# Kernel tuning notes

Measured on AMD Instinct MI355X. Metric: run time of the kernel, lower is better.

## Reference

```python
import jax, jax.numpy as jnp
import numpy as np

B, T, N, C, H = 32, 50, 1024, 128, 64


def setup_inputs() -> dict:
    key = jax.random.key(0)
    ks = jax.random.split(key, 5)
    s_ih = 1.0 / np.sqrt(H)
    return {
        "chars": jax.random.normal(ks[0], (B, T, N, C), dtype=jnp.float32),
        "W_ih": jax.random.uniform(ks[1], (3 * H, C), minval=-s_ih, maxval=s_ih, dtype=jnp.float32),
        "W_hh": jax.random.uniform(ks[2], (3 * H, H), minval=-s_ih, maxval=s_ih, dtype=jnp.float32),
        "b_ih": jax.random.uniform(ks[3], (3 * H,), minval=-s_ih, maxval=s_ih, dtype=jnp.float32),
        "b_hh": jax.random.uniform(ks[4], (3 * H,), minval=-s_ih, maxval=s_ih, dtype=jnp.float32),
    }


def _gru_scan(chars, W_ih, W_hh, b_ih, b_hh):
    b, t, n, c = chars.shape
    h_dim = W_hh.shape[1]
    # (B,T,N,C) -> (T, B*N, C): every (batch, stock) pair is an independent sequence
    x = jnp.transpose(chars, (1, 0, 2, 3)).reshape(t, b * n, c)
    # precompute input projections for all steps: (T, B*N, 3H)
    gi = jnp.einsum("tbc,gc->tbg", x, W_ih) + b_ih

    def step(h, gi_t):
        gh = h @ W_hh.T + b_hh                      # (B*N, 3H)
        i_r, i_z, i_n = jnp.split(gi_t, 3, axis=-1)
        h_r, h_z, h_n = jnp.split(gh, 3, axis=-1)
        r = jax.nn.sigmoid(i_r + h_r)
        z = jax.nn.sigmoid(i_z + h_z)
        nn_ = jnp.tanh(i_n + r * h_n)
        h_new = (1.0 - z) * nn_ + z * h
        return h_new, None

    h0 = jnp.zeros((b * n, h_dim), dtype=chars.dtype)
    h_final, _ = jax.lax.scan(step, h0, gi)
    return h_final.reshape(b, n, h_dim)


def reference(chars, W_ih, W_hh, b_ih, b_hh):
    return _gru_scan(chars, W_ih, W_hh, b_ih, b_hh)
```

## Files before the change

### kernel.cpp

```cpp
#include <hip/hip_runtime.h>


typedef _Float16 half8 __attribute__((ext_vector_type(8)));
typedef float f32x4 __attribute__((ext_vector_type(4)));

constexpr int T_ = 50, N_ = 1024, C_ = 128, H_ = 64;
constexpr int WIH_OFF = 0;
constexpr int WHH_OFF = 49152;
constexpr int H_OFF   = 73728;
constexpr int LDS_BYTES = 90112;

__global__ void prep_weights(const float* __restrict__ Wih, const float* __restrict__ Whh,
                             _Float16* __restrict__ w16) {
  int i = blockIdx.x * 256 + threadIdx.x;
  if (i < 192 * 128) w16[i] = (_Float16)Wih[i];
  if (i < 192 * 64)  w16[24576 + i] = (_Float16)Whh[i];
}

__global__ __launch_bounds__(512, 2) void gru_mfma(
    const float* __restrict__ x, const _Float16* __restrict__ w16,
    const float* __restrict__ bih, const float* __restrict__ bhh,
    float* __restrict__ out)
{
  __shared__ __align__(16) char lds[LDS_BYTES];
  const int tid = threadIdx.x;

  {
    const _Float16* wih = w16;
    const _Float16* whh = w16 + 24576;
#pragma unroll
    for (int rep = 0; rep < 6; ++rep) {
      int i = tid + rep * 512;
      int row = i >> 4;
      uint32_t byte = ((uint32_t)i << 4) ^ ((row & 7) << 4);
      *(half8*)(lds + WIH_OFF + byte) = *(const half8*)(wih + i * 8);
    }
#pragma unroll
    for (int rep = 0; rep < 3; ++rep) {
      int i = tid + rep * 512;
      int row = i >> 3;
      uint32_t byte = ((uint32_t)i << 4) ^ ((row & 7) << 4);
      *(half8*)(lds + WHH_OFF + byte) = *(const half8*)(whh + i * 8);
    }
    half8 zz = {};
#pragma unroll
    for (int rep = 0; rep < 2; ++rep)
      *(half8*)(lds + H_OFF + (tid + rep * 512) * 16) = zz;
  }
  __syncthreads();

  const int wv = tid >> 6, lane = tid & 63;
  const int c = lane & 15, g = lane >> 4;
  const uint32_t hbase = H_OFF + wv * 2048;
  const int gseq0 = blockIdx.x * 128 + wv * 16;
  const int b = gseq0 >> 10, n0 = gseq0 & (N_ - 1);
  const float* xrow = x + ((size_t)b * T_ * N_ + n0 + c) * C_;
  const size_t stepstride = (size_t)N_ * C_;

  float br[4], bz[4], bin[4], bhn[4];
#pragma unroll
  for (int j4 = 0; j4 < 4; ++j4) {
    int j = j4 * 16 + c;
    br[j4]  = bih[j] + bhh[j];
    bz[j4]  = bih[64 + j] + bhh[64 + j];
    bin[j4] = bih[128 + j];
    bhn[j4] = bhh[128 + j];
  }

  float hreg[16];
#pragma unroll
  for (int i = 0; i < 16; ++i) hreg[i] = 0.f;

  float4 raw[8];
#pragma unroll
  for (int ks = 0; ks < 4; ++ks)
#pragma unroll
    for (int hf = 0; hf < 2; ++hf)
      raw[ks * 2 + hf] = *(const float4*)(xrow + ks * 32 + g * 8 + hf * 4);

  for (int t = 0; t < T_; ++t) {
    half8 xf[4];
#pragma unroll
    for (int ks = 0; ks < 4; ++ks) {
      const float4 lo = raw[ks * 2], hi = raw[ks * 2 + 1];
      xf[ks][0] = (_Float16)lo.x; xf[ks][1] = (_Float16)lo.y;
      xf[ks][2] = (_Float16)lo.z; xf[ks][3] = (_Float16)lo.w;
      xf[ks][4] = (_Float16)hi.x; xf[ks][5] = (_Float16)hi.y;
      xf[ks][6] = (_Float16)hi.z; xf[ks][7] = (_Float16)hi.w;
    }
    {
      const int tn = (t + 1 < T_) ? t + 1 : T_ - 1;
      const float* xp = xrow + (size_t)tn * stepstride;
#pragma unroll
      for (int ks = 0; ks < 4; ++ks)
#pragma unroll
        for (int hf = 0; hf < 2; ++hf)
          raw[ks * 2 + hf] = *(const float4*)(xp + ks * 32 + g * 8 + hf * 4);
    }

    f32x4 Orz[8], Oin[4], Ohn[4];
#pragma unroll
    for (int i = 0; i < 8; ++i) Orz[i] = (f32x4){0.f, 0.f, 0.f, 0.f};
#pragma unroll
    for (int i = 0; i < 4; ++i) { Oin[i] = (f32x4){0.f, 0.f, 0.f, 0.f};
                                  Ohn[i] = (f32x4){0.f, 0.f, 0.f, 0.f}; }

#pragma unroll
    for (int ks = 0; ks < 4; ++ks) {
      const half8 a = xf[ks];
#pragma unroll
      for (int ct = 0; ct < 8; ++ct) {
        const int row = ct * 16 + c;
        const uint32_t byte = (uint32_t)(WIH_OFF + row * 256 + ks * 64 + g * 16) ^ ((row & 7) << 4);
        Orz[ct] = __builtin_amdgcn_mfma_f32_16x16x32_f16(a, *(const half8*)(lds + byte), Orz[ct], 0, 0, 0);
      }
#pragma unroll
      for (int ct = 0; ct < 4; ++ct) {
        const int row = 128 + ct * 16 + c;
        const uint32_t byte = (uint32_t)(WIH_OFF + row * 256 + ks * 64 + g * 16) ^ ((row & 7) << 4);
        Oin[ct] = __builtin_amdgcn_mfma_f32_16x16x32_f16(a, *(const half8*)(lds + byte), Oin[ct], 0, 0, 0);
      }
    }
#pragma unroll
    for (int ks2 = 0; ks2 < 2; ++ks2) {
      const uint32_t abyte = (hbase + c * 128 + ks2 * 64 + g * 16) ^ ((c & 7) << 4);
      const half8 a = *(const half8*)(lds + abyte);
#pragma unroll
      for (int ct = 0; ct < 8; ++ct) {
        const int row = ct * 16 + c;
        const uint32_t byte = (uint32_t)(WHH_OFF + row * 128 + ks2 * 64 + g * 16) ^ ((row & 7) << 4);
        Orz[ct] = __builtin_amdgcn_mfma_f32_16x16x32_f16(a, *(const half8*)(lds + byte), Orz[ct], 0, 0, 0);
      }
#pragma unroll
      for (int ct = 0; ct < 4; ++ct) {
        const int row = 128 + ct * 16 + c;
        const uint32_t byte = (uint32_t)(WHH_OFF + row * 128 + ks2 * 64 + g * 16) ^ ((row & 7) << 4);
        Ohn[ct] = __builtin_amdgcn_mfma_f32_16x16x32_f16(a, *(const half8*)(lds + byte), Ohn[ct], 0, 0, 0);
      }
    }

#pragma unroll
    for (int v = 0; v < 4; ++v) {
#pragma unroll
      for (int j4 = 0; j4 < 4; ++j4) {
        const float rp = Orz[j4][v] + br[j4];
        const float zp = Orz[4 + j4][v] + bz[j4];
        const float r = __builtin_amdgcn_rcpf(1.f + __expf(-rp));
        const float z = __builtin_amdgcn_rcpf(1.f + __expf(-zp));
        const float np = Oin[j4][v] + bin[j4] + r * (Ohn[j4][v] + bhn[j4]);
        const float nn = 1.f - 2.f * __builtin_amdgcn_rcpf(__expf(2.f * np) + 1.f);
        const float hn = (1.f - z) * nn + z * hreg[v * 4 + j4];
        hreg[v * 4 + j4] = hn;
        const int s = g * 4 + v;
        const uint32_t byte = (hbase + s * 128 + (j4 * 16 + c) * 2) ^ ((s & 7) << 4);
        *(_Float16*)(lds + byte) = (_Float16)hn;
      }
    }
  }

#pragma unroll
  for (int v = 0; v < 4; ++v) {
    const int s = g * 4 + v;
#pragma unroll
    for (int j4 = 0; j4 < 4; ++j4)
      out[(size_t)(gseq0 + s) * H_ + j4 * 16 + c] = hreg[v * 4 + j4];
  }
}

extern "C" void kernel_launch(void* const* d_in, const int* in_sizes, int n_in,
                              void* d_out, int out_size, void* d_ws, size_t ws_size,
                              hipStream_t stream) {
  const float* chars = (const float*)d_in[0];
  const float* Wih   = (const float*)d_in[1];
  const float* Whh   = (const float*)d_in[2];
  const float* bih   = (const float*)d_in[3];
  const float* bhh   = (const float*)d_in[4];

  _Float16* w16 = (_Float16*)d_ws;

  prep_weights<<<144, 256, 0, stream>>>(Wih, Whh, w16);
  gru_mfma<<<256, 512, 0, stream>>>(chars, w16, bih, bhh, (float*)d_out);
}
```

Before: 252.6 us.

## Switch GRU kernel to 32x32x16 MFMA tiles with W_hh held in registers

Replaces the 16x16x32 MFMA tiling with 32x32x16 MFMAs, so each wave handles 32 sequences. The recurrent weight W_hh moves from LDS into per-lane registers, and the LDS swizzle changes to a 16-way XOR. Blocks shrink to 256 threads with launch bounds of one block per CU, and the next-step input prefetch is placed between MFMA groups. The aim is fewer LDS reads per FLOP and more reuse per instruction, at the cost of higher register pressure and fewer resident waves to hide latency.

```diff
diff --git a/kernel.cpp b/kernel.cpp
--- a/kernel.cpp
+++ b/kernel.cpp
@@ -2,13 +2,12 @@
 
 
 typedef _Float16 half8 __attribute__((ext_vector_type(8)));
-typedef float f32x4 __attribute__((ext_vector_type(4)));
+typedef float f32x16 __attribute__((ext_vector_type(16)));
 
 constexpr int T_ = 50, N_ = 1024, C_ = 128, H_ = 64;
 constexpr int WIH_OFF = 0;
-constexpr int WHH_OFF = 49152;
-constexpr int H_OFF   = 73728;
-constexpr int LDS_BYTES = 90112;
+constexpr int H_OFF   = 49152;
+constexpr int LDS_BYTES = 81920;
 
 __global__ void prep_weights(const float* __restrict__ Wih, const float* __restrict__ Whh,
                              _Float16* __restrict__ w16) {
@@ -17,7 +16,11 @@
   if (i < 192 * 64)  w16[24576 + i] = (_Float16)Whh[i];
 }
 
-__global__ __launch_bounds__(512, 2) void gru_mfma(
+__device__ __forceinline__ float sigm(float x) {
+  return __builtin_amdgcn_rcpf(1.f + __expf(-x));
+}
+
+__global__ __launch_bounds__(256, 1) void gru_mfma32(
     const float* __restrict__ x, const _Float16* __restrict__ w16,
     const float* __restrict__ bih, const float* __restrict__ bhh,
     float* __restrict__ out)
@@ -27,144 +30,161 @@
 
   {
     const _Float16* wih = w16;
-    const _Float16* whh = w16 + 24576;
-#pragma unroll
-    for (int rep = 0; rep < 6; ++rep) {
-      int i = tid + rep * 512;
-      int row = i >> 4;
-      uint32_t byte = ((uint32_t)i << 4) ^ ((row & 7) << 4);
+#pragma unroll
+    for (int rep = 0; rep < 12; ++rep) {
+      int i = tid + rep * 256;
+      int row = i >> 4, gr = i & 15;
+      uint32_t byte = (uint32_t)row * 256 + (uint32_t)((gr ^ (row & 15)) << 4);
       *(half8*)(lds + WIH_OFF + byte) = *(const half8*)(wih + i * 8);
     }
-#pragma unroll
-    for (int rep = 0; rep < 3; ++rep) {
-      int i = tid + rep * 512;
-      int row = i >> 3;
-      uint32_t byte = ((uint32_t)i << 4) ^ ((row & 7) << 4);
-      *(half8*)(lds + WHH_OFF + byte) = *(const half8*)(whh + i * 8);
-    }
     half8 zz = {};
 #pragma unroll
-    for (int rep = 0; rep < 2; ++rep)
-      *(half8*)(lds + H_OFF + (tid + rep * 512) * 16) = zz;
+    for (int rep = 0; rep < 8; ++rep)
+      *(half8*)(lds + H_OFF + tid * 128 + rep * 16) = zz;
   }
   __syncthreads();
 
   const int wv = tid >> 6, lane = tid & 63;
-  const int c = lane & 15, g = lane >> 4;
-  const uint32_t hbase = H_OFF + wv * 2048;
-  const int gseq0 = blockIdx.x * 128 + wv * 16;
+  const int c32 = lane & 31, hf = lane >> 5;
+  const int sw15 = c32 & 15;
+  const uint32_t hbase = H_OFF + wv * 8192;
+  const int gseq0 = blockIdx.x * 128 + wv * 32;
   const int b = gseq0 >> 10, n0 = gseq0 & (N_ - 1);
-  const float* xrow = x + ((size_t)b * T_ * N_ + n0 + c) * C_;
+
+  const _Float16* whh = w16 + 24576;
+  half8 wf[6][4];
+#pragma unroll
+  for (int ct = 0; ct < 6; ++ct)
+#pragma unroll
+    for (int ks = 0; ks < 4; ++ks)
+      wf[ct][ks] = *(const half8*)(whh + (ct * 32 + c32) * 64 + ks * 16 + hf * 8);
+
+  float br[2], bz[2], bin_[2], bhn_[2];
+#pragma unroll
+  for (int jj = 0; jj < 2; ++jj) {
+    int j = jj * 32 + c32;
+    br[jj]   = bih[j] + bhh[j];
+    bz[jj]   = bih[64 + j] + bhh[64 + j];
+    bin_[jj] = bih[128 + j];
+    bhn_[jj] = bhh[128 + j];
+  }
+
+  float hr[32];
+#pragma unroll
+  for (int i = 0; i < 32; ++i) hr[i] = 0.f;
+
+  const float* xlane = x + ((size_t)b * T_ * N_ + n0 + c32) * C_ + hf * 8;
   const size_t stepstride = (size_t)N_ * C_;
 
-  float br[4], bz[4], bin[4], bhn[4];
-#pragma unroll
-  for (int j4 = 0; j4 < 4; ++j4) {
-    int j = j4 * 16 + c;
-    br[j4]  = bih[j] + bhh[j];
-    bz[j4]  = bih[64 + j] + bhh[64 + j];
-    bin[j4] = bih[128 + j];
-    bhn[j4] = bhh[128 + j];
-  }
-
-  float hreg[16];
-#pragma unroll
-  for (int i = 0; i < 16; ++i) hreg[i] = 0.f;
-
-  float4 raw[8];
-#pragma unroll
-  for (int ks = 0; ks < 4; ++ks)
-#pragma unroll
-    for (int hf = 0; hf < 2; ++hf)
-      raw[ks * 2 + hf] = *(const float4*)(xrow + ks * 32 + g * 8 + hf * 4);
+#define WIHB(gt, ks) \
+  (*(const half8*)(lds + WIH_OFF + (uint32_t)(((gt) * 32 + c32) * 256) + \
+                   (uint32_t)(((((ks) * 2 + hf) ^ sw15)) << 4)))
+#define MFMA(a, bfrag, acc) __builtin_amdgcn_mfma_f32_32x32x16_f16((a), (bfrag), (acc), 0, 0, 0)
+
+  float4 raw[16];
+#pragma unroll
+  for (int ks = 0; ks < 8; ++ks) {
+    raw[ks * 2]     = *(const float4*)(xlane + ks * 16);
+    raw[ks * 2 + 1] = *(const float4*)(xlane + ks * 16 + 4);
+  }
 
   for (int t = 0; t < T_; ++t) {
-    half8 xf[4];
+    half8 xf[8];
+#pragma unroll
+    for (int ks = 0; ks < 8; ++ks) {
+      const float4 lo = raw[ks * 2], hi = raw[ks * 2 + 1];
+      half8 v;
+      v[0] = (_Float16)lo.x; v[1] = (_Float16)lo.y;
+      v[2] = (_Float16)lo.z; v[3] = (_Float16)lo.w;
+      v[4] = (_Float16)hi.x; v[5] = (_Float16)hi.y;
+      v[6] = (_Float16)hi.z; v[7] = (_Float16)hi.w;
+      xf[ks] = v;
+    }
+
+    half8 ha[4];
 #pragma unroll
     for (int ks = 0; ks < 4; ++ks) {
-      const float4 lo = raw[ks * 2], hi = raw[ks * 2 + 1];
-      xf[ks][0] = (_Float16)lo.x; xf[ks][1] = (_Float16)lo.y;
-      xf[ks][2] = (_Float16)lo.z; xf[ks][3] = (_Float16)lo.w;
-      xf[ks][4] = (_Float16)hi.x; xf[ks][5] = (_Float16)hi.y;
-      xf[ks][6] = (_Float16)hi.z; xf[ks][7] = (_Float16)hi.w;
-    }
+      uint32_t byte = hbase + (uint32_t)(c32 * 256) + (uint32_t)(((ks * 2 + hf) ^ sw15) << 4);
+      ha[ks] = *(const half8*)(lds + byte);
+    }
+
+    f32x16 aR0 = {}, aZ0 = {}, aN0 = {}, aH0 = {};
+    f32x16 aR1 = {}, aZ1 = {}, aN1 = {}, aH1 = {};
+
+#pragma unroll
+    for (int ks = 0; ks < 8; ++ks) aR0 = MFMA(xf[ks], WIHB(0, ks), aR0);
+#pragma unroll
+    for (int ks = 0; ks < 8; ++ks) aZ0 = MFMA(xf[ks], WIHB(2, ks), aZ0);
+#pragma unroll
+    for (int ks = 0; ks < 8; ++ks) aN0 = MFMA(xf[ks], WIHB(4, ks), aN0);
+#pragma unroll
+    for (int ks = 0; ks < 4; ++ks) aR0 = MFMA(ha[ks], wf[0][ks], aR0);
+#pragma unroll
+    for (int ks = 0; ks < 4; ++ks) aZ0 = MFMA(ha[ks], wf[2][ks], aZ0);
+#pragma unroll
+    for (int ks = 0; ks < 4; ++ks) aH0 = MFMA(ha[ks], wf[4][ks], aH0);
+
+#pragma unroll
+    for (int ks = 0; ks < 8; ++ks) aR1 = MFMA(xf[ks], WIHB(1, ks), aR1);
+#pragma unroll
+    for (int ks = 0; ks < 8; ++ks) aZ1 = MFMA(xf[ks], WIHB(3, ks), aZ1);
+#pragma unroll
+    for (int ks = 0; ks < 8; ++ks) aN1 = MFMA(xf[ks], WIHB(5, ks), aN1);
+
     {
       const int tn = (t + 1 < T_) ? t + 1 : T_ - 1;
-      const float* xp = xrow + (size_t)tn * stepstride;
-#pragma unroll
-      for (int ks = 0; ks < 4; ++ks)
-#pragma unroll
-        for (int hf = 0; hf < 2; ++hf)
-          raw[ks * 2 + hf] = *(const float4*)(xp + ks * 32 + g * 8 + hf * 4);
-    }
-
-    f32x4 Orz[8], Oin[4], Ohn[4];
-#pragma unroll
-    for (int i = 0; i < 8; ++i) Orz[i] = (f32x4){0.f, 0.f, 0.f, 0.f};
-#pragma unroll
-    for (int i = 0; i < 4; ++i) { Oin[i] = (f32x4){0.f, 0.f, 0.f, 0.f};
-                                  Ohn[i] = (f32x4){0.f, 0.f, 0.f, 0.f}; }
-
-#pragma unroll
-    for (int ks = 0; ks < 4; ++ks) {
-      const half8 a = xf[ks];
-#pragma unroll
-      for (int ct = 0; ct < 8; ++ct) {
-        const int row = ct * 16 + c;
-        const uint32_t byte = (uint32_t)(WIH_OFF + row * 256 + ks * 64 + g * 16) ^ ((row & 7) << 4);
-        Orz[ct] = __builtin_amdgcn_mfma_f32_16x16x32_f16(a, *(const half8*)(lds + byte), Orz[ct], 0, 0, 0);
+      const float* xp = xlane + (size_t)tn * stepstride;
+#pragma unroll
+      for (int ks = 0; ks < 8; ++ks) {
+        raw[ks * 2]     = *(const float4*)(xp + ks * 16);
+        raw[ks * 2 + 1] = *(const float4*)(xp + ks * 16 + 4);
       }
-#pragma unroll
-      for (int ct = 0; ct < 4; ++ct) {
-        const int row = 128 + ct * 16 + c;
-        const uint32_t byte = (uint32_t)(WIH_OFF + row * 256 + ks * 64 + g * 16) ^ ((row & 7) << 4);
-        Oin[ct] = __builtin_amdgcn_mfma_f32_16x16x32_f16(a, *(const half8*)(lds + byte), Oin[ct], 0, 0, 0);
-      }
-    }
-#pragma unroll
-    for (int ks2 = 0; ks2 < 2; ++ks2) {
-      const uint32_t abyte = (hbase + c * 128 + ks2 * 64 + g * 16) ^ ((c & 7) << 4);
-      const half8 a = *(const half8*)(lds + abyte);
-#pragma unroll
-      for (int ct = 0; ct < 8; ++ct) {
-        const int row = ct * 16 + c;
-        const uint32_t byte = (uint32_t)(WHH_OFF + row * 128 + ks2 * 64 + g * 16) ^ ((row & 7) << 4);
-        Orz[ct] = __builtin_amdgcn_mfma_f32_16x16x32_f16(a, *(const half8*)(lds + byte), Orz[ct], 0, 0, 0);
-      }
-#pragma unroll
-      for (int ct = 0; ct < 4; ++ct) {
-        const int row = 128 + ct * 16 + c;
-        const uint32_t byte = (uint32_t)(WHH_OFF + row * 128 + ks2 * 64 + g * 16) ^ ((row & 7) << 4);
-        Ohn[ct] = __builtin_amdgcn_mfma_f32_16x16x32_f16(a, *(const half8*)(lds + byte), Ohn[ct], 0, 0, 0);
-      }
-    }
-
-#pragma unroll
-    for (int v = 0; v < 4; ++v) {
-#pragma unroll
-      for (int j4 = 0; j4 < 4; ++j4) {
-        const float rp = Orz[j4][v] + br[j4];
-        const float zp = Orz[4 + j4][v] + bz[j4];
-        const float r = __builtin_amdgcn_rcpf(1.f + __expf(-rp));
-        const float z = __builtin_amdgcn_rcpf(1.f + __expf(-zp));
-        const float np = Oin[j4][v] + bin[j4] + r * (Ohn[j4][v] + bhn[j4]);
-        const float nn = 1.f - 2.f * __builtin_amdgcn_rcpf(__expf(2.f * np) + 1.f);
-        const float hn = (1.f - z) * nn + z * hreg[v * 4 + j4];
-        hreg[v * 4 + j4] = hn;
-        const int s = g * 4 + v;
-        const uint32_t byte = (hbase + s * 128 + (j4 * 16 + c) * 2) ^ ((s & 7) << 4);
-        *(_Float16*)(lds + byte) = (_Float16)hn;
-      }
-    }
-  }
-
-#pragma unroll
-  for (int v = 0; v < 4; ++v) {
-    const int s = g * 4 + v;
-#pragma unroll
-    for (int j4 = 0; j4 < 4; ++j4)
-      out[(size_t)(gseq0 + s) * H_ + j4 * 16 + c] = hreg[v * 4 + j4];
-  }
+    }
+
+#pragma unroll
+    for (int ks = 0; ks < 4; ++ks) aR1 = MFMA(ha[ks], wf[1][ks], aR1);
+#pragma unroll
+    for (int ks = 0; ks < 4; ++ks) aZ1 = MFMA(ha[ks], wf[3][ks], aZ1);
+#pragma unroll
+    for (int ks = 0; ks < 4; ++ks) aH1 = MFMA(ha[ks], wf[5][ks], aH1);
+
+#pragma unroll
+    for (int rg = 0; rg < 16; ++rg) {
+      const int seq = (rg & 3) + 8 * (rg >> 2) + 4 * hf;
+      const float r = sigm(aR0[rg] + br[0]);
+      const float z = sigm(aZ0[rg] + bz[0]);
+      const float np = aN0[rg] + bin_[0] + r * (aH0[rg] + bhn_[0]);
+      const float nn = 1.f - 2.f * __builtin_amdgcn_rcpf(__expf(2.f * np) + 1.f);
+      const float hn = (1.f - z) * nn + z * hr[rg];
+      hr[rg] = hn;
+      const uint32_t gr = (uint32_t)((0 * 4 + (c32 >> 3)) ^ (seq & 15));
+      const uint32_t byte = hbase + (uint32_t)(seq * 256) + (gr << 4) + (uint32_t)((c32 * 2) & 15);
+      *(_Float16*)(lds + byte) = (_Float16)hn;
+    }
+#pragma unroll
+    for (int rg = 0; rg < 16; ++rg) {
+      const int seq = (rg & 3) + 8 * (rg >> 2) + 4 * hf;
+      const float r = sigm(aR1[rg] + br[1]);
+      const float z = sigm(aZ1[rg] + bz[1]);
+      const float np = aN1[rg] + bin_[1] + r * (aH1[rg] + bhn_[1]);
+      const float nn = 1.f - 2.f * __builtin_amdgcn_rcpf(__expf(2.f * np) + 1.f);
+      const float hn = (1.f - z) * nn + z * hr[16 + rg];
+      hr[16 + rg] = hn;
+      const uint32_t gr = (uint32_t)((1 * 4 + (c32 >> 3)) ^ (seq & 15));
+      const uint32_t byte = hbase + (uint32_t)(seq * 256) + (gr << 4) + (uint32_t)((c32 * 2) & 15);
+      *(_Float16*)(lds + byte) = (_Float16)hn;
+    }
+  }
+
+#pragma unroll
+  for (int jj = 0; jj < 2; ++jj)
+#pragma unroll
+    for (int rg = 0; rg < 16; ++rg) {
+      const int seq = (rg & 3) + 8 * (rg >> 2) + 4 * hf;
+      out[(size_t)(gseq0 + seq) * H_ + jj * 32 + c32] = hr[jj * 16 + rg];
+    }
+#undef WIHB
+#undef MFMA
 }
 
 extern "C" void kernel_launch(void* const* d_in, const int* in_sizes, int n_in,
@@ -179,5 +199,5 @@
   _Float16* w16 = (_Float16*)d_ws;
 
   prep_weights<<<144, 256, 0, stream>>>(Wih, Whh, w16);
-  gru_mfma<<<256, 512, 0, stream>>>(chars, w16, bih, bhh, (float*)d_out);
-}
+  gru_mfma32<<<256, 256, 0, stream>>>(chars, w16, bih, bhh, (float*)d_out);
+}
```

Measured after the change: 231.7 us. 8.3% less time.

## Keep W_hh fragments in registers and halve block size for GRU kernel

Applied to the files above, without the earlier changes.

Loads the recurrent weight matrix W_hh once per wave into register-resident half8 fragments instead of re-reading it from LDS every timestep. This shrinks LDS per block so the kernel can run as 512 blocks of 256 threads, each covering 64 sequences. The per-step LDS traffic on the serial recurrence path should drop. The cost is much higher VGPR pressure, which could cause spills or limit occupancy.

```diff
diff --git a/kernel.cpp b/kernel.cpp
--- a/kernel.cpp
+++ b/kernel.cpp
@@ -5,10 +5,9 @@
 typedef float f32x4 __attribute__((ext_vector_type(4)));
 
 constexpr int T_ = 50, N_ = 1024, C_ = 128, H_ = 64;
-constexpr int WIH_OFF = 0;
-constexpr int WHH_OFF = 49152;
-constexpr int H_OFF   = 73728;
-constexpr int LDS_BYTES = 90112;
+constexpr uint32_t WIH_OFF = 0;
+constexpr uint32_t HT_OFF  = 49152;
+constexpr int LDS_BYTES = 57344;
 
 __global__ void prep_weights(const float* __restrict__ Wih, const float* __restrict__ Whh,
                              _Float16* __restrict__ w16) {
@@ -17,7 +16,11 @@
   if (i < 192 * 64)  w16[24576 + i] = (_Float16)Whh[i];
 }
 
-__global__ __launch_bounds__(512, 2) void gru_mfma(
+__device__ __forceinline__ float sigm(float x) {
+  return __builtin_amdgcn_rcpf(1.f + __expf(-x));
+}
+
+__global__ __launch_bounds__(256, 2) void gru_tlp(
     const float* __restrict__ x, const _Float16* __restrict__ w16,
     const float* __restrict__ bih, const float* __restrict__ bhh,
     float* __restrict__ out)
@@ -26,145 +29,144 @@
   const int tid = threadIdx.x;
 
   {
-    const _Float16* wih = w16;
-    const _Float16* whh = w16 + 24576;
 #pragma unroll
-    for (int rep = 0; rep < 6; ++rep) {
-      int i = tid + rep * 512;
+    for (int rep = 0; rep < 12; ++rep) {
+      int i = tid + rep * 256;
       int row = i >> 4;
-      uint32_t byte = ((uint32_t)i << 4) ^ ((row & 7) << 4);
-      *(half8*)(lds + WIH_OFF + byte) = *(const half8*)(wih + i * 8);
-    }
-#pragma unroll
-    for (int rep = 0; rep < 3; ++rep) {
-      int i = tid + rep * 512;
-      int row = i >> 3;
-      uint32_t byte = ((uint32_t)i << 4) ^ ((row & 7) << 4);
-      *(half8*)(lds + WHH_OFF + byte) = *(const half8*)(whh + i * 8);
+      uint32_t byte = ((uint32_t)i << 4) ^ ((uint32_t)(row & 7) << 4);
+      *(half8*)(lds + WIH_OFF + byte) = *(const half8*)(w16 + i * 8);
     }
     half8 zz = {};
-#pragma unroll
-    for (int rep = 0; rep < 2; ++rep)
-      *(half8*)(lds + H_OFF + (tid + rep * 512) * 16) = zz;
+    *(half8*)(lds + HT_OFF + tid * 32)      = zz;
+    *(half8*)(lds + HT_OFF + tid * 32 + 16) = zz;
   }
   __syncthreads();
 
   const int wv = tid >> 6, lane = tid & 63;
   const int c = lane & 15, g = lane >> 4;
-  const uint32_t hbase = H_OFF + wv * 2048;
-  const int gseq0 = blockIdx.x * 128 + wv * 16;
-  const int b = gseq0 >> 10, n0 = gseq0 & (N_ - 1);
-  const float* xrow = x + ((size_t)b * T_ * N_ + n0 + c) * C_;
-  const size_t stepstride = (size_t)N_ * C_;
+  const int sw7 = c & 7;
+  const uint32_t ht = HT_OFF + (uint32_t)wv * 2048;
+  const int seq0 = blockIdx.x * 64 + wv * 16;
+  const int b = seq0 >> 10, n0 = seq0 & (N_ - 1);
 
-  float br[4], bz[4], bin[4], bhn[4];
+  const _Float16* whh = w16 + 24576;
+  half8 wf[12][2];
+#pragma unroll
+  for (int jt = 0; jt < 12; ++jt)
+#pragma unroll
+    for (int ks2 = 0; ks2 < 2; ++ks2)
+      wf[jt][ks2] = *(const half8*)(whh + (jt * 16 + c) * 64 + ks2 * 32 + g * 8);
+
+  float br[4], bz[4], bin_[4], bhn_[4];
 #pragma unroll
   for (int j4 = 0; j4 < 4; ++j4) {
     int j = j4 * 16 + c;
-    br[j4]  = bih[j] + bhh[j];
-    bz[j4]  = bih[64 + j] + bhh[64 + j];
-    bin[j4] = bih[128 + j];
-    bhn[j4] = bhh[128 + j];
+    br[j4]   = bih[j] + bhh[j];
+    bz[j4]   = bih[64 + j] + bhh[64 + j];
+    bin_[j4] = bih[128 + j];
+    bhn_[j4] = bhh[128 + j];
   }
 
-  float hreg[16];
+  float hr[16];
 #pragma unroll
-  for (int i = 0; i < 16; ++i) hreg[i] = 0.f;
+  for (int i = 0; i < 16; ++i) hr[i] = 0.f;
+
+  const float* xlane = x + ((size_t)b * T_ * N_ + n0 + c) * C_ + g * 8;
+  const size_t stepstride = (size_t)N_ * C_;
+
+#define WIHB(jt, ks) \
+  (*(const half8*)(lds + WIH_OFF + (uint32_t)(((jt) * 16 + c) * 256) + \
+                   (uint32_t)((((ks) * 4 + g) ^ sw7) << 4)))
+#define MFMA16(a, bf, acc) __builtin_amdgcn_mfma_f32_16x16x32_f16((a), (bf), (acc), 0, 0, 0)
 
   float4 raw[8];
 #pragma unroll
-  for (int ks = 0; ks < 4; ++ks)
-#pragma unroll
-    for (int hf = 0; hf < 2; ++hf)
-      raw[ks * 2 + hf] = *(const float4*)(xrow + ks * 32 + g * 8 + hf * 4);
+  for (int ks = 0; ks < 4; ++ks) {
+    raw[ks * 2]     = *(const float4*)(xlane + ks * 32);
+    raw[ks * 2 + 1] = *(const float4*)(xlane + ks * 32 + 4);
+  }
 
   for (int t = 0; t < T_; ++t) {
     half8 xf[4];
 #pragma unroll
     for (int ks = 0; ks < 4; ++ks) {
       const float4 lo = raw[ks * 2], hi = raw[ks * 2 + 1];
-      xf[ks][0] = (_Float16)lo.x; xf[ks][1] = (_Float16)lo.y;
-      xf[ks][2] = (_Float16)lo.z; xf[ks][3] = (_Float16)lo.w;
-      xf[ks][4] = (_Float16)hi.x; xf[ks][5] = (_Float16)hi.y;
-      xf[ks][6] = (_Float16)hi.z; xf[ks][7] = (_Float16)hi.w;
+      half8 v;
+      v[0] = (_Float16)lo.x; v[1] = (_Float16)lo.y;
+      v[2] = (_Float16)lo.z; v[3] = (_Float16)lo.w;
+      v[4] = (_Float16)hi.x; v[5] = (_Float16)hi.y;
+      v[6] = (_Float16)hi.z; v[7] = (_Float16)hi.w;
+      xf[ks] = v;
     }
     {
       const int tn = (t + 1 < T_) ? t + 1 : T_ - 1;
-      const float* xp = xrow + (size_t)tn * stepstride;
+      const float* xp = xlane + (size_t)tn * stepstride;
 #pragma unroll
-      for (int ks = 0; ks < 4; ++ks)
+      for (int ks = 0; ks < 4; ++ks) {
+        raw[ks * 2]     = *(const float4*)(xp + ks * 32);
+        raw[ks * 2 + 1] = *(const float4*)(xp + ks * 32 + 4);
+      }
+    }
+    half8 ha[2];
 #pragma unroll
-        for (int hf = 0; hf < 2; ++hf)
-          raw[ks * 2 + hf] = *(const float4*)(xp + ks * 32 + g * 8 + hf * 4);
+    for (int ks2 = 0; ks2 < 2; ++ks2)
+      ha[ks2] = *(const half8*)(lds + ht + (uint32_t)c * 128 +
+                                (uint32_t)(((ks2 * 4 + g) ^ sw7) << 4));
+
+    f32x4 aR[4], aZ[4], aN[4], aH[4];
+#pragma unroll
+    for (int j4 = 0; j4 < 4; ++j4) {
+      aR[j4] = (f32x4){0.f, 0.f, 0.f, 0.f}; aZ[j4] = (f32x4){0.f, 0.f, 0.f, 0.f};
+      aN[j4] = (f32x4){0.f, 0.f, 0.f, 0.f}; aH[j4] = (f32x4){0.f, 0.f, 0.f, 0.f};
     }
-
-    f32x4 Orz[8], Oin[4], Ohn[4];
-#pragma unroll
-    for (int i = 0; i < 8; ++i) Orz[i] = (f32x4){0.f, 0.f, 0.f, 0.f};
-#pragma unroll
-    for (int i = 0; i < 4; ++i) { Oin[i] = (f32x4){0.f, 0.f, 0.f, 0.f};
-                                  Ohn[i] = (f32x4){0.f, 0.f, 0.f, 0.f}; }
 
 #pragma unroll
     for (int ks = 0; ks < 4; ++ks) {
       const half8 a = xf[ks];
 #pragma unroll
-      for (int ct = 0; ct < 8; ++ct) {
-        const int row = ct * 16 + c;
-        const uint32_t byte = (uint32_t)(WIH_OFF + row * 256 + ks * 64 + g * 16) ^ ((row & 7) << 4);
-        Orz[ct] = __builtin_amdgcn_mfma_f32_16x16x32_f16(a, *(const half8*)(lds + byte), Orz[ct], 0, 0, 0);
-      }
+      for (int j4 = 0; j4 < 4; ++j4) aR[j4] = MFMA16(a, WIHB(j4, ks),     aR[j4]);
 #pragma unroll
-      for (int ct = 0; ct < 4; ++ct) {
-        const int row = 128 + ct * 16 + c;
-        const uint32_t byte = (uint32_t)(WIH_OFF + row * 256 + ks * 64 + g * 16) ^ ((row & 7) << 4);
-        Oin[ct] = __builtin_amdgcn_mfma_f32_16x16x32_f16(a, *(const half8*)(lds + byte), Oin[ct], 0, 0, 0);
-      }
-    }
+      for (int j4 = 0; j4 < 4; ++j4) aZ[j4] = MFMA16(a, WIHB(4 + j4, ks), aZ[j4]);
 #pragma unroll
-    for (int ks2 = 0; ks2 < 2; ++ks2) {
-      const uint32_t abyte = (hbase + c * 128 + ks2 * 64 + g * 16) ^ ((c & 7) << 4);
-      const half8 a = *(const half8*)(lds + abyte);
-#pragma unroll
-      for (int ct = 0; ct < 8; ++ct) {
-        const int row = ct * 16 + c;
-        const uint32_t byte = (uint32_t)(WHH_OFF + row * 128 + ks2 * 64 + g * 16) ^ ((row & 7) << 4);
-        Orz[ct] = __builtin_amdgcn_mfma_f32_16x16x32_f16(a, *(const half8*)(lds + byte), Orz[ct], 0, 0, 0);
-      }
-#pragma unroll
-      for (int ct = 0; ct < 4; ++ct) {
-        const int row = 128 + ct * 16 + c;
-        const uint32_t byte = (uint32_t)(WHH_OFF + row * 128 + ks2 * 64 + g * 16) ^ ((row & 7) << 4);
-        Ohn[ct] = __builtin_amdgcn_mfma_f32_16x16x32_f16(a, *(const half8*)(lds + byte), Ohn[ct], 0, 0, 0);
-      }
+      for (int j4 = 0; j4 < 4; ++j4) aN[j4] = MFMA16(a, WIHB(8 + j4, ks), aN[j4]);
     }
 
 #pragma unroll
-    for (int v = 0; v < 4; ++v) {
+    for (int ks2 = 0; ks2 < 2; ++ks2) {
+      const half8 a = ha[ks2];
 #pragma unroll
-      for (int j4 = 0; j4 < 4; ++j4) {
-        const float rp = Orz[j4][v] + br[j4];
-        const float zp = Orz[4 + j4][v] + bz[j4];
-        const float r = __builtin_amdgcn_rcpf(1.f + __expf(-rp));
-        const float z = __builtin_amdgcn_rcpf(1.f + __expf(-zp));
-        const float np = Oin[j4][v] + bin[j4] + r * (Ohn[j4][v] + bhn[j4]);
+      for (int j4 = 0; j4 < 4; ++j4) aR[j4] = MFMA16(a, wf[j4][ks2],     aR[j4]);
+#pragma unroll
+      for (int j4 = 0; j4 < 4; ++j4) aZ[j4] = MFMA16(a, wf[4 + j4][ks2], aZ[j4]);
+#pragma unroll
+      for (int j4 = 0; j4 < 4; ++j4) aH[j4] = MFMA16(a, wf[8 + j4][ks2], aH[j4]);
+    }
+
+#pragma unroll
+    for (int j4 = 0; j4 < 4; ++j4) {
+#pragma unroll
+      for (int v = 0; v < 4; ++v) {
+        const float r = sigm(aR[j4][v] + br[j4]);
+        const float z = sigm(aZ[j4][v] + bz[j4]);
+        const float np = aN[j4][v] + bin_[j4] + r * (aH[j4][v] + bhn_[j4]);
         const float nn = 1.f - 2.f * __builtin_amdgcn_rcpf(__expf(2.f * np) + 1.f);
-        const float hn = (1.f - z) * nn + z * hreg[v * 4 + j4];
-        hreg[v * 4 + j4] = hn;
-        const int s = g * 4 + v;
-        const uint32_t byte = (hbase + s * 128 + (j4 * 16 + c) * 2) ^ ((s & 7) << 4);
+        const float hn = (1.f - z) * nn + z * hr[j4 * 4 + v];
+        hr[j4 * 4 + v] = hn;
+        const int seq = g * 4 + v;
+        const uint32_t gr = (uint32_t)((j4 * 2 + (c >> 3)) ^ (seq & 7));
+        const uint32_t byte = ht + (uint32_t)seq * 128 + (gr << 4) + (uint32_t)((c & 7) * 2);
         *(_Float16*)(lds + byte) = (_Float16)hn;
       }
     }
   }
 
 #pragma unroll
-  for (int v = 0; v < 4; ++v) {
-    const int s = g * 4 + v;
+  for (int j4 = 0; j4 < 4; ++j4)
 #pragma unroll
-    for (int j4 = 0; j4 < 4; ++j4)
-      out[(size_t)(gseq0 + s) * H_ + j4 * 16 + c] = hreg[v * 4 + j4];
-  }
+    for (int v = 0; v < 4; ++v)
+      out[(size_t)(seq0 + g * 4 + v) * H_ + j4 * 16 + c] = hr[j4 * 4 + v];
+#undef WIHB
+#undef MFMA16
 }
 
 extern "C" void kernel_launch(void* const* d_in, const int* in_sizes, int n_in,
@@ -178,6 +180,6 @@
 
   _Float16* w16 = (_Float16*)d_ws;
 
-  prep_weights<<<144, 256, 0, stream>>>(Wih, Whh, w16);
-  gru_mfma<<<256, 512, 0, stream>>>(chars, w16, bih, bhh, (float*)d_out);
+  prep_weights<<<96, 256, 0, stream>>>(Wih, Whh, w16);
+  gru_tlp<<<512, 256, 0, stream>>>(chars, w16, bih, bhh, (float*)d_out);
 }
```

Result: slower. 260.4 us (+3.1%).
